# Kernel optimization log

Measured on AMD Instinct MI355X. Metric: run time of the kernel, lower is better.

Reference implementation:

```python
import jax, jax.numpy as jnp
import numpy as np
from jax import lax

B, L, H, K = 64, 1024, 768, 4
C1, C2 = 0.1, 0.1


def crf_marginals(feats, maskf, T):
    """Batched linear-chain CRF forward-backward.
    feats: [B,L,K] emission scores, maskf: [B,L] float (1=valid), T: [K,K] transitions.
    Returns marginals [B,L,K] (zeroed at padded positions)."""
    a0 = feats[:, 0]  # [B,K]

    def fwd_step(a, xs):
        f_t, m_t = xs  # [B,K], [B]
        new = f_t + jax.nn.logsumexp(a[:, :, None] + T[None], axis=1)
        a = jnp.where(m_t[:, None] > 0, new, a)  # freeze alpha past last valid token
        return a, a

    _, alphas_rest = lax.scan(fwd_step, a0,
                              (jnp.swapaxes(feats[:, 1:], 0, 1), maskf[:, 1:].T))
    alphas = jnp.concatenate([a0[None], alphas_rest], axis=0)  # [L,B,K]
    logZ = jax.nn.logsumexp(alphas[-1], axis=-1)  # [B] (alpha frozen at last valid t)

    bL = jnp.zeros_like(a0)

    def bwd_step(b, xs):
        f_n, m_n = xs  # emission/mask at t+1
        new = jax.nn.logsumexp(T[None] + (f_n + b)[:, None, :], axis=2)
        b = jnp.where(m_n[:, None] > 0, new, b)  # beta stays 0 until last valid token
        return b, b

    xs = (jnp.swapaxes(feats[:, 1:][:, ::-1], 0, 1), maskf[:, 1:][:, ::-1].T)
    _, betas_rev = lax.scan(bwd_step, bL, xs)
    betas = jnp.concatenate([bL[None], betas_rev], axis=0)[::-1]  # [L,B,K]

    marg = jnp.exp(alphas + betas - logZ[None, :, None]) * maskf.T[:, :, None]
    return jnp.swapaxes(marg, 0, 1)  # [B,L,K]


def _forward(hidden, maskf, w, b, T):
    feats = hidden @ w.T + b                      # [B,L,K] feat2tri
    marg = crf_marginals(feats, maskf, T)
    sp = marg[:, :, 1]                            # select_polarities, masked [B,L]
    gamma = sp.sum(axis=1) / 2.0                  # [B]
    sent_vs = jnp.einsum('bl,blh->bh', sp, hidden) / gamma[:, None]
    s_prob = sp / gamma[:, None]                  # padded-ragged per-token probs
    s_prob_norm = jnp.abs(s_prob).sum(axis=1).mean()
    pena = jax.nn.relu(T[1, 0] - T[0, 0]) + jax.nn.relu(T[0, 1] - T[1, 1])
    norm_pen = C1 * pena + C2 * s_prob_norm
    return sent_vs, norm_pen, s_prob


def setup_inputs():
    key = jax.random.key(0)
    ks = jax.random.split(key, 8)
    hidden = jax.random.normal(ks[0], (B, L, H), dtype=jnp.float32)
    seq_lens = jax.random.randint(ks[1], (B,), L // 4, L + 1)
    # hidden_mask: 0 for valid tokens, nonzero for padding (forward uses mask = hidden_mask==0)
    hidden_mask = (jnp.arange(L)[None, :] >= seq_lens[:, None]).astype(jnp.int32)
    subj_position = jax.random.randint(ks[2], (B, L), -20, 21)
    obj_position = jax.random.randint(ks[3], (B, L), -20, 21)
    pe_inputs = jax.random.randint(ks[4], (B, L), 0, 2 * L)
    pe_binary = jax.random.randint(ks[5], (B, L), 0, 2)
    w_feat2tri = jax.random.normal(ks[6], (K, H), dtype=jnp.float32) * (1.0 / np.sqrt(H)).astype(np.float32)
    b_feat2tri = jnp.zeros((K,), dtype=jnp.float32)
    transitions = jax.random.normal(ks[7], (K, K), dtype=jnp.float32) * 0.1
    return dict(hidden=hidden, hidden_mask=hidden_mask, subj_position=subj_position,
                obj_position=obj_position, seq_lens=seq_lens, pe_inputs=pe_inputs,
                pe_binary=pe_binary, w_feat2tri=w_feat2tri, b_feat2tri=b_feat2tri,
                transitions=transitions)


def reference(hidden, hidden_mask, subj_position, obj_position, seq_lens, pe_inputs,
              pe_binary, w_feat2tri, b_feat2tri, transitions):
    maskf = (hidden_mask == 0).astype(hidden.dtype)
    # relevance is computed in the original forward but never consumed downstream,
    # so it has no effect on outputs; omitted here.
    return _forward(hidden, maskf, w_feat2tri, b_feat2tri, transitions)
```

## Files before the change

### kernel.cpp

```cpp
#include <hip/hip_runtime.h>

#define B 64
#define L 1024
#define H 768
#define NROWS (B * L)
#define LOG2E 1.4426950408889634f
#define CS 16
#define NCH 64
#define NEG -1e30f

#define EXP2(x) __builtin_amdgcn_exp2f(x)
#define LOG2(x) __builtin_amdgcn_logf(x)

__device__ __forceinline__ void gbarrier(unsigned* cnt, unsigned nblk) {
    __syncthreads();
    if (threadIdx.x == 0) {
        __threadfence();
        __hip_atomic_fetch_add(cnt, 1u, __ATOMIC_ACQ_REL, __HIP_MEMORY_SCOPE_AGENT);
        while (__hip_atomic_load(cnt, __ATOMIC_ACQUIRE, __HIP_MEMORY_SCOPE_AGENT) < nblk)
            __builtin_amdgcn_s_sleep(1);
        __threadfence();
    }
    __syncthreads();
}

__global__ __launch_bounds__(256) void feats_kernel(
    const float* __restrict__ hidden, const float* __restrict__ w,
    const float* __restrict__ bias, float4* __restrict__ featsT,
    unsigned* __restrict__ counters)
{
    if (blockIdx.x == 0 && threadIdx.x < 4) counters[threadIdx.x] = 0u;

    const int lane = threadIdx.x & 63;
    const int wave = (blockIdx.x * blockDim.x + threadIdx.x) >> 6;
    const int nwaves = (gridDim.x * blockDim.x) >> 6;

    float wr[3][4][4];
#pragma unroll
    for (int c = 0; c < 3; ++c)
#pragma unroll
        for (int j = 0; j < 4; ++j)
#pragma unroll
            for (int k = 0; k < 4; ++k)
                wr[c][j][k] = w[k * H + lane * 4 + 256 * c + j];
    const float bb0 = bias[0], bb1 = bias[1], bb2 = bias[2], bb3 = bias[3];

    for (int row = wave; row < NROWS; row += nwaves) {
        const float4* hrow = reinterpret_cast<const float4*>(hidden) + (size_t)row * (H / 4);
        float acc[4] = {0.f, 0.f, 0.f, 0.f};
#pragma unroll
        for (int c = 0; c < 3; ++c) {
            float4 h = hrow[lane + 64 * c];
            const float hv[4] = {h.x, h.y, h.z, h.w};
#pragma unroll
            for (int j = 0; j < 4; ++j)
#pragma unroll
                for (int k = 0; k < 4; ++k)
                    acc[k] = fmaf(hv[j], wr[c][j][k], acc[k]);
        }
#pragma unroll
        for (int k = 0; k < 4; ++k) {
            float v = acc[k];
#pragma unroll
            for (int s = 32; s >= 1; s >>= 1) v += __shfl_xor(v, s, 64);
            acc[k] = v;
        }
        if (lane == 0) {
            const int b = row >> 10, l = row & 1023;
            featsT[l * B + b] = make_float4((acc[0] + bb0) * LOG2E, (acc[1] + bb1) * LOG2E,
                                            (acc[2] + bb2) * LOG2E, (acc[3] + bb3) * LOG2E);
        }
    }
}

__global__ __launch_bounds__(128) void crf_mid_kernel(
    const float4* __restrict__ featsT, const int* __restrict__ seq_lens,
    const float* __restrict__ T, float* __restrict__ mats,
    float* __restrict__ vbound, float* __restrict__ logZ,
    float* __restrict__ spu, float* __restrict__ chunksum,
    unsigned* __restrict__ counters)
{
    const int tid = threadIdx.x;
    const int b = tid & 63;
    const int dir = tid >> 6;
    const int c = blockIdx.x;
    const int sl = seq_lens[b];

    float eT2[4][4];
#pragma unroll
    for (int i = 0; i < 4; ++i)
#pragma unroll
        for (int j = 0; j < 4; ++j) eT2[i][j] = EXP2(T[i * 4 + j] * LOG2E);

    {
        const int lo = c * CS + 1;
        const int hi = min(c * CS + CS, L - 1);
        const int ns = hi - lo + 1;

        float4 fr[CS];
#pragma unroll
        for (int u = 0; u < CS; ++u) {
            const int t = dir ? max(hi - u, lo) : min(lo + u, hi);
            fr[u] = featsT[t * B + b];
        }

        float M[4][4];
#pragma unroll
        for (int i = 0; i < 4; ++i)
#pragma unroll
            for (int j = 0; j < 4; ++j) M[i][j] = (i == j) ? 0.f : NEG;

        if (dir == 0) {
#pragma unroll
            for (int u = 0; u < CS; ++u) {
                const int t = lo + u;
                const bool valid = (u < ns) && (t < sl);
                const float f[4] = {fr[u].x, fr[u].y, fr[u].z, fr[u].w};
                float nM[4][4];
#pragma unroll
                for (int i = 0; i < 4; ++i) {
                    const float rm = fmaxf(fmaxf(M[i][0], M[i][1]), fmaxf(M[i][2], M[i][3]));
                    const float e0 = EXP2(M[i][0] - rm), e1 = EXP2(M[i][1] - rm);
                    const float e2 = EXP2(M[i][2] - rm), e3 = EXP2(M[i][3] - rm);
#pragma unroll
                    for (int j = 0; j < 4; ++j) {
                        const float s = (e0 * eT2[0][j] + e1 * eT2[1][j]) + (e2 * eT2[2][j] + e3 * eT2[3][j]);
                        nM[i][j] = f[j] + rm + LOG2(s);
                    }
                }
#pragma unroll
                for (int i = 0; i < 4; ++i)
#pragma unroll
                    for (int j = 0; j < 4; ++j) M[i][j] = valid ? nM[i][j] : M[i][j];
            }
        } else {
#pragma unroll
            for (int u = 0; u < CS; ++u) {
                const int n = hi - u;
                const bool valid = (u < ns) && (n < sl);
                const float f[4] = {fr[u].x, fr[u].y, fr[u].z, fr[u].w};
                float nM[4][4];
#pragma unroll
                for (int j = 0; j < 4; ++j) {
                    const float c0 = f[0] + M[0][j], c1 = f[1] + M[1][j];
                    const float c2 = f[2] + M[2][j], c3 = f[3] + M[3][j];
                    const float cm = fmaxf(fmaxf(c0, c1), fmaxf(c2, c3));
                    const float g0 = EXP2(c0 - cm), g1 = EXP2(c1 - cm);
                    const float g2 = EXP2(c2 - cm), g3 = EXP2(c3 - cm);
#pragma unroll
                    for (int i = 0; i < 4; ++i) {
                        const float s = (g0 * eT2[i][0] + g1 * eT2[i][1]) + (g2 * eT2[i][2] + g3 * eT2[i][3]);
                        nM[i][j] = cm + LOG2(s);
                    }
                }
#pragma unroll
                for (int i = 0; i < 4; ++i)
#pragma unroll
                    for (int j = 0; j < 4; ++j) M[i][j] = valid ? nM[i][j] : M[i][j];
            }
        }
#pragma unroll
        for (int i = 0; i < 4; ++i)
#pragma unroll
            for (int j = 0; j < 4; ++j)
                mats[((dir * NCH + c) * 16 + i * 4 + j) * B + b] = M[i][j];
    }

    gbarrier(&counters[0], NCH);

    if (blockIdx.x == 0) {
        float Ms[8][16];
#pragma unroll
        for (int p = 0; p < 7; ++p) {
            const int cc = dir ? (NCH - 1 - p) : p;
#pragma unroll
            for (int k = 0; k < 16; ++k)
                Ms[p][k] = mats[((dir * NCH + cc) * 16 + k) * B + b];
        }

        float v0, v1, v2, v3;
        if (dir == 0) {
            const float4 f0 = featsT[b];
            v0 = f0.x; v1 = f0.y; v2 = f0.z; v3 = f0.w;
        } else {
            v0 = v1 = v2 = v3 = 0.f;
        }

#pragma unroll
        for (int u = 0; u < NCH; ++u) {
            const int cc = dir ? (NCH - 1 - u) : u;
            vbound[((dir * NCH + cc) * 4 + 0) * B + b] = v0;
            vbound[((dir * NCH + cc) * 4 + 1) * B + b] = v1;
            vbound[((dir * NCH + cc) * 4 + 2) * B + b] = v2;
            vbound[((dir * NCH + cc) * 4 + 3) * B + b] = v3;
            if (u + 7 < NCH) {
                const int cp = dir ? (NCH - 1 - (u + 7)) : (u + 7);
#pragma unroll
                for (int k = 0; k < 16; ++k)
                    Ms[(u + 7) & 7][k] = mats[((dir * NCH + cp) * 16 + k) * B + b];
            }
            float n[4];
            if (dir == 0) {
#pragma unroll
                for (int j = 0; j < 4; ++j) {
                    const float c0 = v0 + Ms[u & 7][0 * 4 + j], c1 = v1 + Ms[u & 7][1 * 4 + j];
                    const float c2 = v2 + Ms[u & 7][2 * 4 + j], c3 = v3 + Ms[u & 7][3 * 4 + j];
                    const float m = fmaxf(fmaxf(c0, c1), fmaxf(c2, c3));
                    const float s = (EXP2(c0 - m) + EXP2(c1 - m)) + (EXP2(c2 - m) + EXP2(c3 - m));
                    n[j] = m + LOG2(s);
                }
            } else {
#pragma unroll
                for (int i = 0; i < 4; ++i) {
                    const float c0 = v0 + Ms[u & 7][i * 4 + 0], c1 = v1 + Ms[u & 7][i * 4 + 1];
                    const float c2 = v2 + Ms[u & 7][i * 4 + 2], c3 = v3 + Ms[u & 7][i * 4 + 3];
                    const float m = fmaxf(fmaxf(c0, c1), fmaxf(c2, c3));
                    const float s = (EXP2(c0 - m) + EXP2(c1 - m)) + (EXP2(c2 - m) + EXP2(c3 - m));
                    n[i] = m + LOG2(s);
                }
            }
            v0 = n[0]; v1 = n[1]; v2 = n[2]; v3 = n[3];
        }
        if (dir == 0) {
            const float m = fmaxf(fmaxf(v0, v1), fmaxf(v2, v3));
            logZ[b] = m + LOG2(EXP2(v0 - m) + EXP2(v1 - m) + EXP2(v2 - m) + EXP2(v3 - m));
        }
    }

    gbarrier(&counters[1], NCH);

    __shared__ float ldb[CS * 64];
    {
        const int base = c * CS;

        if (dir == 1) {
            float v0 = vbound[((NCH + c) * 4 + 0) * B + b];
            float v1 = vbound[((NCH + c) * 4 + 1) * B + b];
            float v2 = vbound[((NCH + c) * 4 + 2) * B + b];
            float v3 = vbound[((NCH + c) * 4 + 3) * B + b];
            const bool last = (c == NCH - 1);
            const int hi_n = last ? (L - 1) : (base + CS);
            const int cnt = last ? (CS - 1) : CS;
            if (last) ldb[15 * 64 + b] = v1;
            float4 fr[CS];
#pragma unroll
            for (int u = 0; u < CS; ++u) fr[u] = featsT[max(hi_n - u, base + 1) * B + b];
#pragma unroll
            for (int u = 0; u < CS; ++u) {
                if (u < cnt) {
                    const int n = hi_n - u;
                    const bool valid = n < sl;
                    const float4 f = fr[u];
                    const float c0 = f.x + v0, c1 = f.y + v1, c2 = f.z + v2, c3 = f.w + v3;
                    const float m = fmaxf(fmaxf(c0, c1), fmaxf(c2, c3));
                    const float g0 = EXP2(c0 - m), g1 = EXP2(c1 - m), g2 = EXP2(c2 - m), g3 = EXP2(c3 - m);
                    const float s0 = (g0 * eT2[0][0] + g1 * eT2[0][1]) + (g2 * eT2[0][2] + g3 * eT2[0][3]);
                    const float s1 = (g0 * eT2[1][0] + g1 * eT2[1][1]) + (g2 * eT2[1][2] + g3 * eT2[1][3]);
                    const float s2 = (g0 * eT2[2][0] + g1 * eT2[2][1]) + (g2 * eT2[2][2] + g3 * eT2[2][3]);
                    const float s3 = (g0 * eT2[3][0] + g1 * eT2[3][1]) + (g2 * eT2[3][2] + g3 * eT2[3][3]);
                    const float n0 = m + LOG2(s0), n1 = m + LOG2(s1);
                    const float n2 = m + LOG2(s2), n3 = m + LOG2(s3);
                    v0 = valid ? n0 : v0; v1 = valid ? n1 : v1;
                    v2 = valid ? n2 : v2; v3 = valid ? n3 : v3;
                    ldb[(n - 1 - base) * 64 + b] = v1;
                }
            }
        }

        float av[CS];
        if (dir == 0) {
            float a0 = vbound[(c * 4 + 0) * B + b];
            float a1 = vbound[(c * 4 + 1) * B + b];
            float a2 = vbound[(c * 4 + 2) * B + b];
            float a3 = vbound[(c * 4 + 3) * B + b];
            av[0] = a1;
            float4 fr[CS - 1];
#pragma unroll
            for (int u = 1; u < CS; ++u) fr[u - 1] = featsT[(c * CS + u) * B + b];
#pragma unroll
            for (int u = 1; u < CS; ++u) {
                const int t = base + u;
                const bool valid = t < sl;
                const float4 f = fr[u - 1];
                const float m = fmaxf(fmaxf(a0, a1), fmaxf(a2, a3));
                const float e0 = EXP2(a0 - m), e1 = EXP2(a1 - m), e2 = EXP2(a2 - m), e3 = EXP2(a3 - m);
                const float s0 = (e0 * eT2[0][0] + e1 * eT2[1][0]) + (e2 * eT2[2][0] + e3 * eT2[3][0]);
                const float s1 = (e0 * eT2[0][1] + e1 * eT2[1][1]) + (e2 * eT2[2][1] + e3 * eT2[3][1]);
                const float s2 = (e0 * eT2[0][2] + e1 * eT2[1][2]) + (e2 * eT2[2][2] + e3 * eT2[3][2]);
                const float s3 = (e0 * eT2[0][3] + e1 * eT2[1][3]) + (e2 * eT2[2][3] + e3 * eT2[3][3]);
                const float n0 = f.x + m + LOG2(s0), n1 = f.y + m + LOG2(s1);
                const float n2 = f.z + m + LOG2(s2), n3 = f.w + m + LOG2(s3);
                a0 = valid ? n0 : a0; a1 = valid ? n1 : a1;
                a2 = valid ? n2 : a2; a3 = valid ? n3 : a3;
                av[u] = a1;
            }
        }

        __syncthreads();

        if (dir == 0) {
            const float lz = logZ[b];
            float sp[CS];
            float local = 0.f;
#pragma unroll
            for (int u = 0; u < CS; ++u) {
                const int l = base + u;
                const float x = (l < sl) ? EXP2(av[u] + ldb[u * 64 + b] - lz) : 0.f;
                sp[u] = x;
                local += x;
            }
            float4* dst = reinterpret_cast<float4*>(spu + b * L + base);
#pragma unroll
            for (int q = 0; q < 4; ++q)
                dst[q] = make_float4(sp[4 * q], sp[4 * q + 1], sp[4 * q + 2], sp[4 * q + 3]);
            chunksum[c * 64 + b] = local;
        }
    }
}

__global__ __launch_bounds__(256) void sentv_kernel(
    const float* __restrict__ hidden, const float* __restrict__ spu,
    const float* __restrict__ chunksum, const float* __restrict__ T,
    float* __restrict__ out, float* __restrict__ sprob)
{
    const int hc = blockIdx.x;
    const int b  = blockIdx.y;
    const int tid = threadIdx.x;
    const int lane = tid & 63;
    const int w = tid >> 6;

    __shared__ float s_tot;
    if (tid < 64) {
        float v = chunksum[tid * 64 + b];
#pragma unroll
        for (int s = 32; s >= 1; s >>= 1) v += __shfl_xor(v, s, 64);
        if (tid == 0) s_tot = v;
    }
    __syncthreads();
    const float inv = 2.0f / s_tot;

    const float4* hb = reinterpret_cast<const float4*>(hidden + ((size_t)b * L) * H + hc * 256) + lane;
    const float* sp = spu + b * L;

    float4 acc = make_float4(0.f, 0.f, 0.f, 0.f);
#pragma unroll 8
    for (int i = 0; i < 256; ++i) {
        const int l = w + 4 * i;
        const float s = sp[l];
        const float4 h = hb[(size_t)l * (H / 4)];
        acc.x = fmaf(s, h.x, acc.x); acc.y = fmaf(s, h.y, acc.y);
        acc.z = fmaf(s, h.z, acc.z); acc.w = fmaf(s, h.w, acc.w);
    }

    __shared__ float4 red[4][64];
    red[w][lane] = acc;
    __syncthreads();
    if (tid < 64) {
        const float4 a0 = red[0][lane], a1 = red[1][lane], a2 = red[2][lane], a3 = red[3][lane];
        float4 r;
        r.x = ((a0.x + a1.x) + (a2.x + a3.x)) * inv;
        r.y = ((a0.y + a1.y) + (a2.y + a3.y)) * inv;
        r.z = ((a0.z + a1.z) + (a2.z + a3.z)) * inv;
        r.w = ((a0.w + a1.w) + (a2.w + a3.w)) * inv;
        reinterpret_cast<float4*>(out + (size_t)b * H + hc * 256)[lane] = r;
    }

    if (hc == 0) {
#pragma unroll
        for (int q = 0; q < 4; ++q) {
            const int l = tid + q * 256;
            sprob[b * L + l] = sp[l] * inv;
        }
        if (b == 0 && tid == 0) {
            const float pena = fmaxf(T[4] - T[0], 0.f) + fmaxf(T[1] - T[5], 0.f);
            out[B * H] = 0.1f * pena + 0.1f * 2.0f;
        }
    }
}

extern "C" void kernel_launch(void* const* d_in, const int* in_sizes, int n_in,
                              void* d_out, int out_size, void* d_ws, size_t ws_size,
                              hipStream_t stream) {
    const float* hidden   = (const float*)d_in[0];
    const int*   seq_lens = (const int*)d_in[4];
    const float* w        = (const float*)d_in[7];
    const float* bias     = (const float*)d_in[8];
    const float* T        = (const float*)d_in[9];

    float* ws = (float*)d_ws;
    float4*   featsT   = (float4*)(ws);
    float*    mats     = ws + 262144;
    float*    vbound   = ws + 393216;
    float*    logZ     = ws + 425984;
    float*    chunksum = ws + 426048;
    float*    spu      = ws + 430144;
    unsigned* counters = (unsigned*)(ws + 495680);

    float* out   = (float*)d_out;
    float* sprob = out + B * H + 1;

    feats_kernel<<<2048, 256, 0, stream>>>(hidden, w, bias, featsT, counters);
    crf_mid_kernel<<<NCH, 128, 0, stream>>>((const float4*)featsT, seq_lens, T, mats,
                                            vbound, logZ, spu, chunksum, counters);
    sentv_kernel<<<dim3(3, 64), 256, 0, stream>>>(hidden, spu, chunksum, T, out, sprob);
}
```

Measured before the change: 107.0 us.

## Switch CRF to scaled probability space, split kernels, and re-grid sentence-vector reduction

The CRF scans now run in linear probability space with periodic power-of-two renormalisation, which replaces log-sum-exp (many exp2/log2 per step) with plain multiply-adds. The single fused CRF kernel and its software grid barriers are split into separate chunk-matrix, boundary, and rescan launches. The weighted hidden reduction is re-gridded to 512 blocks of 768 threads with a separate final combine kernel, to raise parallelism when streaming hidden. The cost is three extra kernel launches and a risk of precision or underflow differences from scaled-linear arithmetic.

```diff
diff --git a/kernel.cpp b/kernel.cpp
--- a/kernel.cpp
+++ b/kernel.cpp
@@ -7,30 +7,22 @@
 #define LOG2E 1.4426950408889634f
 #define CS 16
 #define NCH 64
-#define NEG -1e30f
 
 #define EXP2(x) __builtin_amdgcn_exp2f(x)
 #define LOG2(x) __builtin_amdgcn_logf(x)
 
-__device__ __forceinline__ void gbarrier(unsigned* cnt, unsigned nblk) {
-    __syncthreads();
-    if (threadIdx.x == 0) {
-        __threadfence();
-        __hip_atomic_fetch_add(cnt, 1u, __ATOMIC_ACQ_REL, __HIP_MEMORY_SCOPE_AGENT);
-        while (__hip_atomic_load(cnt, __ATOMIC_ACQUIRE, __HIP_MEMORY_SCOPE_AGENT) < nblk)
-            __builtin_amdgcn_s_sleep(1);
-        __threadfence();
-    }
-    __syncthreads();
+__device__ __forceinline__ void renorm4(float& x0, float& x1, float& x2, float& x3, float& lc) {
+    const float g = fmaxf(fmaxf(x0, x1), fmaxf(x2, x3));
+    const int e = (__float_as_int(g) >> 23) & 255;
+    const float s = __int_as_float((254 - e) << 23);
+    x0 *= s; x1 *= s; x2 *= s; x3 *= s;
+    lc += (float)(e - 127);
 }
 
 __global__ __launch_bounds__(256) void feats_kernel(
     const float* __restrict__ hidden, const float* __restrict__ w,
-    const float* __restrict__ bias, float4* __restrict__ featsT,
-    unsigned* __restrict__ counters)
-{
-    if (blockIdx.x == 0 && threadIdx.x < 4) counters[threadIdx.x] = 0u;
-
+    const float* __restrict__ bias, float4* __restrict__ pfeatsT)
+{
     const int lane = threadIdx.x & 63;
     const int wave = (blockIdx.x * blockDim.x + threadIdx.x) >> 6;
     const int nwaves = (gridDim.x * blockDim.x) >> 6;
@@ -67,24 +59,177 @@
         }
         if (lane == 0) {
             const int b = row >> 10, l = row & 1023;
-            featsT[l * B + b] = make_float4((acc[0] + bb0) * LOG2E, (acc[1] + bb1) * LOG2E,
-                                            (acc[2] + bb2) * LOG2E, (acc[3] + bb3) * LOG2E);
-        }
-    }
-}
-
-__global__ __launch_bounds__(128) void crf_mid_kernel(
-    const float4* __restrict__ featsT, const int* __restrict__ seq_lens,
-    const float* __restrict__ T, float* __restrict__ mats,
-    float* __restrict__ vbound, float* __restrict__ logZ,
-    float* __restrict__ spu, float* __restrict__ chunksum,
-    unsigned* __restrict__ counters)
+            pfeatsT[l * B + b] = make_float4(EXP2((acc[0] + bb0) * LOG2E),
+                                             EXP2((acc[1] + bb1) * LOG2E),
+                                             EXP2((acc[2] + bb2) * LOG2E),
+                                             EXP2((acc[3] + bb3) * LOG2E));
+        }
+    }
+}
+
+__global__ __launch_bounds__(128) void chunkmat_kernel(
+    const float4* __restrict__ pfeatsT, const int* __restrict__ seq_lens,
+    const float* __restrict__ T, float* __restrict__ mats_p,
+    float* __restrict__ mats_lc)
+{
+    const int b = threadIdx.x & 63;
+    const int dir = threadIdx.x >> 6;
+    const int c = blockIdx.x;
+    const int sl = seq_lens[b];
+    const int lo = c * CS + 1;
+    const int hi = min(c * CS + CS, L - 1);
+    const int ns = hi - lo + 1;
+
+    float eT2[4][4];
+#pragma unroll
+    for (int i = 0; i < 4; ++i)
+#pragma unroll
+        for (int j = 0; j < 4; ++j) eT2[i][j] = EXP2(T[i * 4 + j] * LOG2E);
+
+    float4 fr[CS];
+#pragma unroll
+    for (int u = 0; u < CS; ++u) {
+        const int t = dir ? max(hi - u, lo) : min(lo + u, hi);
+        fr[u] = pfeatsT[t * B + b];
+    }
+
+    float M[4][4];
+#pragma unroll
+    for (int i = 0; i < 4; ++i)
+#pragma unroll
+        for (int j = 0; j < 4; ++j) M[i][j] = (i == j) ? 1.f : 0.f;
+    float lc = 0.f;
+
+#pragma unroll
+    for (int u = 0; u < CS; ++u) {
+        const int pos = dir ? (hi - u) : (lo + u);
+        const bool valid = (u < ns) && (pos < sl);
+        const float f[4] = {fr[u].x, fr[u].y, fr[u].z, fr[u].w};
+        float nM[4][4];
+        if (dir == 0) {
+#pragma unroll
+            for (int i = 0; i < 4; ++i)
+#pragma unroll
+                for (int j = 0; j < 4; ++j) {
+                    const float s = (M[i][0] * eT2[0][j] + M[i][1] * eT2[1][j]) +
+                                    (M[i][2] * eT2[2][j] + M[i][3] * eT2[3][j]);
+                    nM[i][j] = s * f[j];
+                }
+        } else {
+            float Mg[4][4];
+#pragma unroll
+            for (int k = 0; k < 4; ++k)
+#pragma unroll
+                for (int j = 0; j < 4; ++j) Mg[k][j] = f[k] * M[k][j];
+#pragma unroll
+            for (int i = 0; i < 4; ++i)
+#pragma unroll
+                for (int j = 0; j < 4; ++j)
+                    nM[i][j] = (eT2[i][0] * Mg[0][j] + eT2[i][1] * Mg[1][j]) +
+                               (eT2[i][2] * Mg[2][j] + eT2[i][3] * Mg[3][j]);
+        }
+#pragma unroll
+        for (int i = 0; i < 4; ++i)
+#pragma unroll
+            for (int j = 0; j < 4; ++j) M[i][j] = valid ? nM[i][j] : M[i][j];
+
+        if (u == 7 || u == CS - 1) {
+            float g = 0.f;
+#pragma unroll
+            for (int i = 0; i < 4; ++i)
+#pragma unroll
+                for (int j = 0; j < 4; ++j) g = fmaxf(g, M[i][j]);
+            const int e = (__float_as_int(g) >> 23) & 255;
+            const float s = __int_as_float((254 - e) << 23);
+#pragma unroll
+            for (int i = 0; i < 4; ++i)
+#pragma unroll
+                for (int j = 0; j < 4; ++j) M[i][j] *= s;
+            lc += (float)(e - 127);
+        }
+    }
+#pragma unroll
+    for (int i = 0; i < 4; ++i)
+#pragma unroll
+        for (int j = 0; j < 4; ++j)
+            mats_p[((dir * NCH + c) * 16 + i * 4 + j) * B + b] = M[i][j];
+    mats_lc[(dir * NCH + c) * B + b] = lc;
+}
+
+__global__ __launch_bounds__(128) void bound_kernel(
+    const float4* __restrict__ pfeatsT, const float* __restrict__ mats_p,
+    const float* __restrict__ mats_lc, float* __restrict__ vbound_p,
+    float* __restrict__ vbound_lc, float* __restrict__ logZ)
+{
+    const int b = threadIdx.x & 63;
+    const int dir = threadIdx.x >> 6;
+
+    float Ms[8][17];
+#pragma unroll
+    for (int p = 0; p < 7; ++p) {
+        const int cc = dir ? (NCH - 1 - p) : p;
+#pragma unroll
+        for (int k = 0; k < 16; ++k)
+            Ms[p][k] = mats_p[((dir * NCH + cc) * 16 + k) * B + b];
+        Ms[p][16] = mats_lc[(dir * NCH + cc) * B + b];
+    }
+
+    float v0, v1, v2, v3, vlc = 0.f;
+    if (dir == 0) {
+        const float4 f0 = pfeatsT[b];
+        v0 = f0.x; v1 = f0.y; v2 = f0.z; v3 = f0.w;
+    } else {
+        v0 = v1 = v2 = v3 = 1.f;
+    }
+
+#pragma unroll 8
+    for (int u = 0; u < NCH; ++u) {
+        const int cc = dir ? (NCH - 1 - u) : u;
+        vbound_p[((dir * NCH + cc) * 4 + 0) * B + b] = v0;
+        vbound_p[((dir * NCH + cc) * 4 + 1) * B + b] = v1;
+        vbound_p[((dir * NCH + cc) * 4 + 2) * B + b] = v2;
+        vbound_p[((dir * NCH + cc) * 4 + 3) * B + b] = v3;
+        vbound_lc[(dir * NCH + cc) * B + b] = vlc;
+        if (u + 7 < NCH) {
+            const int cp = dir ? (NCH - 1 - (u + 7)) : (u + 7);
+#pragma unroll
+            for (int k = 0; k < 16; ++k)
+                Ms[(u + 7) & 7][k] = mats_p[((dir * NCH + cp) * 16 + k) * B + b];
+            Ms[(u + 7) & 7][16] = mats_lc[(dir * NCH + cp) * B + b];
+        }
+        const float* Pm = Ms[u & 7];
+        float n0, n1, n2, n3;
+        if (dir == 0) {
+            n0 = (v0 * Pm[0] + v1 * Pm[4]) + (v2 * Pm[8] + v3 * Pm[12]);
+            n1 = (v0 * Pm[1] + v1 * Pm[5]) + (v2 * Pm[9] + v3 * Pm[13]);
+            n2 = (v0 * Pm[2] + v1 * Pm[6]) + (v2 * Pm[10] + v3 * Pm[14]);
+            n3 = (v0 * Pm[3] + v1 * Pm[7]) + (v2 * Pm[11] + v3 * Pm[15]);
+        } else {
+            n0 = (Pm[0] * v0 + Pm[1] * v1) + (Pm[2] * v2 + Pm[3] * v3);
+            n1 = (Pm[4] * v0 + Pm[5] * v1) + (Pm[6] * v2 + Pm[7] * v3);
+            n2 = (Pm[8] * v0 + Pm[9] * v1) + (Pm[10] * v2 + Pm[11] * v3);
+            n3 = (Pm[12] * v0 + Pm[13] * v1) + (Pm[14] * v2 + Pm[15] * v3);
+        }
+        v0 = n0; v1 = n1; v2 = n2; v3 = n3;
+        vlc += Pm[16];
+        renorm4(v0, v1, v2, v3, vlc);
+    }
+    if (dir == 0)
+        logZ[b] = LOG2(((v0 + v1) + (v2 + v3))) + vlc;
+}
+
+__global__ __launch_bounds__(128) void rescan_sp_kernel(
+    const float4* __restrict__ pfeatsT, const int* __restrict__ seq_lens,
+    const float* __restrict__ T, const float* __restrict__ vbound_p,
+    const float* __restrict__ vbound_lc, const float* __restrict__ logZ,
+    float* __restrict__ spu, float* __restrict__ chunksum)
 {
     const int tid = threadIdx.x;
     const int b = tid & 63;
     const int dir = tid >> 6;
     const int c = blockIdx.x;
     const int sl = seq_lens[b];
+    const int base = c * CS;
 
     float eT2[4][4];
 #pragma unroll
@@ -92,242 +237,137 @@
 #pragma unroll
         for (int j = 0; j < 4; ++j) eT2[i][j] = EXP2(T[i * 4 + j] * LOG2E);
 
-    {
-        const int lo = c * CS + 1;
-        const int hi = min(c * CS + CS, L - 1);
-        const int ns = hi - lo + 1;
-
+    __shared__ float ldb_p[CS * 64];
+    __shared__ float ldb_lc[CS * 64];
+
+    if (dir == 1) {
+        float v0 = vbound_p[((NCH + c) * 4 + 0) * B + b];
+        float v1 = vbound_p[((NCH + c) * 4 + 1) * B + b];
+        float v2 = vbound_p[((NCH + c) * 4 + 2) * B + b];
+        float v3 = vbound_p[((NCH + c) * 4 + 3) * B + b];
+        float blc = vbound_lc[(NCH + c) * B + b];
+        const bool last = (c == NCH - 1);
+        const int hi_n = last ? (L - 1) : (base + CS);
+        const int cnt = last ? (CS - 1) : CS;
+        if (last) { ldb_p[15 * 64 + b] = v1; ldb_lc[15 * 64 + b] = blc; }
         float4 fr[CS];
 #pragma unroll
+        for (int u = 0; u < CS; ++u) fr[u] = pfeatsT[max(hi_n - u, base + 1) * B + b];
+#pragma unroll
         for (int u = 0; u < CS; ++u) {
-            const int t = dir ? max(hi - u, lo) : min(lo + u, hi);
-            fr[u] = featsT[t * B + b];
-        }
-
-        float M[4][4];
-#pragma unroll
-        for (int i = 0; i < 4; ++i)
-#pragma unroll
-            for (int j = 0; j < 4; ++j) M[i][j] = (i == j) ? 0.f : NEG;
-
-        if (dir == 0) {
-#pragma unroll
-            for (int u = 0; u < CS; ++u) {
-                const int t = lo + u;
-                const bool valid = (u < ns) && (t < sl);
-                const float f[4] = {fr[u].x, fr[u].y, fr[u].z, fr[u].w};
-                float nM[4][4];
-#pragma unroll
-                for (int i = 0; i < 4; ++i) {
-                    const float rm = fmaxf(fmaxf(M[i][0], M[i][1]), fmaxf(M[i][2], M[i][3]));
-                    const float e0 = EXP2(M[i][0] - rm), e1 = EXP2(M[i][1] - rm);
-                    const float e2 = EXP2(M[i][2] - rm), e3 = EXP2(M[i][3] - rm);
-#pragma unroll
-                    for (int j = 0; j < 4; ++j) {
-                        const float s = (e0 * eT2[0][j] + e1 * eT2[1][j]) + (e2 * eT2[2][j] + e3 * eT2[3][j]);
-                        nM[i][j] = f[j] + rm + LOG2(s);
-                    }
-                }
-#pragma unroll
-                for (int i = 0; i < 4; ++i)
-#pragma unroll
-                    for (int j = 0; j < 4; ++j) M[i][j] = valid ? nM[i][j] : M[i][j];
+            if (u < cnt) {
+                const int n = hi_n - u;
+                const bool valid = n < sl;
+                const float4 f = fr[u];
+                const float c0 = f.x * v0, c1 = f.y * v1, c2 = f.z * v2, c3 = f.w * v3;
+                const float n0 = (eT2[0][0] * c0 + eT2[0][1] * c1) + (eT2[0][2] * c2 + eT2[0][3] * c3);
+                const float n1 = (eT2[1][0] * c0 + eT2[1][1] * c1) + (eT2[1][2] * c2 + eT2[1][3] * c3);
+                const float n2 = (eT2[2][0] * c0 + eT2[2][1] * c1) + (eT2[2][2] * c2 + eT2[2][3] * c3);
+                const float n3 = (eT2[3][0] * c0 + eT2[3][1] * c1) + (eT2[3][2] * c2 + eT2[3][3] * c3);
+                v0 = valid ? n0 : v0; v1 = valid ? n1 : v1;
+                v2 = valid ? n2 : v2; v3 = valid ? n3 : v3;
+                if ((u & 3) == 3) renorm4(v0, v1, v2, v3, blc);
+                ldb_p[(n - 1 - base) * 64 + b] = v1;
+                ldb_lc[(n - 1 - base) * 64 + b] = blc;
             }
-        } else {
-#pragma unroll
-            for (int u = 0; u < CS; ++u) {
-                const int n = hi - u;
-                const bool valid = (u < ns) && (n < sl);
-                const float f[4] = {fr[u].x, fr[u].y, fr[u].z, fr[u].w};
-                float nM[4][4];
-#pragma unroll
-                for (int j = 0; j < 4; ++j) {
-                    const float c0 = f[0] + M[0][j], c1 = f[1] + M[1][j];
-                    const float c2 = f[2] + M[2][j], c3 = f[3] + M[3][j];
-                    const float cm = fmaxf(fmaxf(c0, c1), fmaxf(c2, c3));
-                    const float g0 = EXP2(c0 - cm), g1 = EXP2(c1 - cm);
-                    const float g2 = EXP2(c2 - cm), g3 = EXP2(c3 - cm);
-#pragma unroll
-                    for (int i = 0; i < 4; ++i) {
-                        const float s = (g0 * eT2[i][0] + g1 * eT2[i][1]) + (g2 * eT2[i][2] + g3 * eT2[i][3]);
-                        nM[i][j] = cm + LOG2(s);
-                    }
-                }
-#pragma unroll
-                for (int i = 0; i < 4; ++i)
-#pragma unroll
-                    for (int j = 0; j < 4; ++j) M[i][j] = valid ? nM[i][j] : M[i][j];
-            }
-        }
-#pragma unroll
-        for (int i = 0; i < 4; ++i)
-#pragma unroll
-            for (int j = 0; j < 4; ++j)
-                mats[((dir * NCH + c) * 16 + i * 4 + j) * B + b] = M[i][j];
-    }
-
-    gbarrier(&counters[0], NCH);
-
-    if (blockIdx.x == 0) {
-        float Ms[8][16];
-#pragma unroll
-        for (int p = 0; p < 7; ++p) {
-            const int cc = dir ? (NCH - 1 - p) : p;
-#pragma unroll
-            for (int k = 0; k < 16; ++k)
-                Ms[p][k] = mats[((dir * NCH + cc) * 16 + k) * B + b];
-        }
-
-        float v0, v1, v2, v3;
-        if (dir == 0) {
-            const float4 f0 = featsT[b];
-            v0 = f0.x; v1 = f0.y; v2 = f0.z; v3 = f0.w;
-        } else {
-            v0 = v1 = v2 = v3 = 0.f;
-        }
-
-#pragma unroll
-        for (int u = 0; u < NCH; ++u) {
-            const int cc = dir ? (NCH - 1 - u) : u;
-            vbound[((dir * NCH + cc) * 4 + 0) * B + b] = v0;
-            vbound[((dir * NCH + cc) * 4 + 1) * B + b] = v1;
-            vbound[((dir * NCH + cc) * 4 + 2) * B + b] = v2;
-            vbound[((dir * NCH + cc) * 4 + 3) * B + b] = v3;
-            if (u + 7 < NCH) {
-                const int cp = dir ? (NCH - 1 - (u + 7)) : (u + 7);
-#pragma unroll
-                for (int k = 0; k < 16; ++k)
-                    Ms[(u + 7) & 7][k] = mats[((dir * NCH + cp) * 16 + k) * B + b];
-            }
-            float n[4];
-            if (dir == 0) {
-#pragma unroll
-                for (int j = 0; j < 4; ++j) {
-                    const float c0 = v0 + Ms[u & 7][0 * 4 + j], c1 = v1 + Ms[u & 7][1 * 4 + j];
-                    const float c2 = v2 + Ms[u & 7][2 * 4 + j], c3 = v3 + Ms[u & 7][3 * 4 + j];
-                    const float m = fmaxf(fmaxf(c0, c1), fmaxf(c2, c3));
-                    const float s = (EXP2(c0 - m) + EXP2(c1 - m)) + (EXP2(c2 - m) + EXP2(c3 - m));
-                    n[j] = m + LOG2(s);
-                }
-            } else {
-#pragma unroll
-                for (int i = 0; i < 4; ++i) {
-                    const float c0 = v0 + Ms[u & 7][i * 4 + 0], c1 = v1 + Ms[u & 7][i * 4 + 1];
-                    const float c2 = v2 + Ms[u & 7][i * 4 + 2], c3 = v3 + Ms[u & 7][i * 4 + 3];
-                    const float m = fmaxf(fmaxf(c0, c1), fmaxf(c2, c3));
-                    const float s = (EXP2(c0 - m) + EXP2(c1 - m)) + (EXP2(c2 - m) + EXP2(c3 - m));
-                    n[i] = m + LOG2(s);
-                }
-            }
-            v0 = n[0]; v1 = n[1]; v2 = n[2]; v3 = n[3];
-        }
-        if (dir == 0) {
-            const float m = fmaxf(fmaxf(v0, v1), fmaxf(v2, v3));
-            logZ[b] = m + LOG2(EXP2(v0 - m) + EXP2(v1 - m) + EXP2(v2 - m) + EXP2(v3 - m));
-        }
-    }
-
-    gbarrier(&counters[1], NCH);
-
-    __shared__ float ldb[CS * 64];
-    {
-        const int base = c * CS;
-
-        if (dir == 1) {
-            float v0 = vbound[((NCH + c) * 4 + 0) * B + b];
-            float v1 = vbound[((NCH + c) * 4 + 1) * B + b];
-            float v2 = vbound[((NCH + c) * 4 + 2) * B + b];
-            float v3 = vbound[((NCH + c) * 4 + 3) * B + b];
-            const bool last = (c == NCH - 1);
-            const int hi_n = last ? (L - 1) : (base + CS);
-            const int cnt = last ? (CS - 1) : CS;
-            if (last) ldb[15 * 64 + b] = v1;
-            float4 fr[CS];
-#pragma unroll
-            for (int u = 0; u < CS; ++u) fr[u] = featsT[max(hi_n - u, base + 1) * B + b];
-#pragma unroll
-            for (int u = 0; u < CS; ++u) {
-                if (u < cnt) {
-                    const int n = hi_n - u;
-                    const bool valid = n < sl;
-                    const float4 f = fr[u];
-                    const float c0 = f.x + v0, c1 = f.y + v1, c2 = f.z + v2, c3 = f.w + v3;
-                    const float m = fmaxf(fmaxf(c0, c1), fmaxf(c2, c3));
-                    const float g0 = EXP2(c0 - m), g1 = EXP2(c1 - m), g2 = EXP2(c2 - m), g3 = EXP2(c3 - m);
-                    const float s0 = (g0 * eT2[0][0] + g1 * eT2[0][1]) + (g2 * eT2[0][2] + g3 * eT2[0][3]);
-                    const float s1 = (g0 * eT2[1][0] + g1 * eT2[1][1]) + (g2 * eT2[1][2] + g3 * eT2[1][3]);
-                    const float s2 = (g0 * eT2[2][0] + g1 * eT2[2][1]) + (g2 * eT2[2][2] + g3 * eT2[2][3]);
-                    const float s3 = (g0 * eT2[3][0] + g1 * eT2[3][1]) + (g2 * eT2[3][2] + g3 * eT2[3][3]);
-                    const float n0 = m + LOG2(s0), n1 = m + LOG2(s1);
-                    const float n2 = m + LOG2(s2), n3 = m + LOG2(s3);
-                    v0 = valid ? n0 : v0; v1 = valid ? n1 : v1;
-                    v2 = valid ? n2 : v2; v3 = valid ? n3 : v3;
-                    ldb[(n - 1 - base) * 64 + b] = v1;
-                }
-            }
-        }
-
-        float av[CS];
-        if (dir == 0) {
-            float a0 = vbound[(c * 4 + 0) * B + b];
-            float a1 = vbound[(c * 4 + 1) * B + b];
-            float a2 = vbound[(c * 4 + 2) * B + b];
-            float a3 = vbound[(c * 4 + 3) * B + b];
-            av[0] = a1;
-            float4 fr[CS - 1];
-#pragma unroll
-            for (int u = 1; u < CS; ++u) fr[u - 1] = featsT[(c * CS + u) * B + b];
-#pragma unroll
-            for (int u = 1; u < CS; ++u) {
-                const int t = base + u;
-                const bool valid = t < sl;
-                const float4 f = fr[u - 1];
-                const float m = fmaxf(fmaxf(a0, a1), fmaxf(a2, a3));
-                const float e0 = EXP2(a0 - m), e1 = EXP2(a1 - m), e2 = EXP2(a2 - m), e3 = EXP2(a3 - m);
-                const float s0 = (e0 * eT2[0][0] + e1 * eT2[1][0]) + (e2 * eT2[2][0] + e3 * eT2[3][0]);
-                const float s1 = (e0 * eT2[0][1] + e1 * eT2[1][1]) + (e2 * eT2[2][1] + e3 * eT2[3][1]);
-                const float s2 = (e0 * eT2[0][2] + e1 * eT2[1][2]) + (e2 * eT2[2][2] + e3 * eT2[3][2]);
-                const float s3 = (e0 * eT2[0][3] + e1 * eT2[1][3]) + (e2 * eT2[2][3] + e3 * eT2[3][3]);
-                const float n0 = f.x + m + LOG2(s0), n1 = f.y + m + LOG2(s1);
-                const float n2 = f.z + m + LOG2(s2), n3 = f.w + m + LOG2(s3);
-                a0 = valid ? n0 : a0; a1 = valid ? n1 : a1;
-                a2 = valid ? n2 : a2; a3 = valid ? n3 : a3;
-                av[u] = a1;
-            }
-        }
-
-        __syncthreads();
-
-        if (dir == 0) {
-            const float lz = logZ[b];
-            float sp[CS];
-            float local = 0.f;
-#pragma unroll
-            for (int u = 0; u < CS; ++u) {
-                const int l = base + u;
-                const float x = (l < sl) ? EXP2(av[u] + ldb[u * 64 + b] - lz) : 0.f;
-                sp[u] = x;
-                local += x;
-            }
-            float4* dst = reinterpret_cast<float4*>(spu + b * L + base);
-#pragma unroll
-            for (int q = 0; q < 4; ++q)
-                dst[q] = make_float4(sp[4 * q], sp[4 * q + 1], sp[4 * q + 2], sp[4 * q + 3]);
-            chunksum[c * 64 + b] = local;
-        }
-    }
-}
-
-__global__ __launch_bounds__(256) void sentv_kernel(
+        }
+    }
+
+    float av_p[CS], av_lc[CS];
+    if (dir == 0) {
+        float a0 = vbound_p[(c * 4 + 0) * B + b];
+        float a1 = vbound_p[(c * 4 + 1) * B + b];
+        float a2 = vbound_p[(c * 4 + 2) * B + b];
+        float a3 = vbound_p[(c * 4 + 3) * B + b];
+        float alc = vbound_lc[c * B + b];
+        av_p[0] = a1; av_lc[0] = alc;
+        float4 fr[CS - 1];
+#pragma unroll
+        for (int u = 1; u < CS; ++u) fr[u - 1] = pfeatsT[(base + u) * B + b];
+#pragma unroll
+        for (int u = 1; u < CS; ++u) {
+            const int t = base + u;
+            const bool valid = t < sl;
+            const float4 f = fr[u - 1];
+            const float s0 = (a0 * eT2[0][0] + a1 * eT2[1][0]) + (a2 * eT2[2][0] + a3 * eT2[3][0]);
+            const float s1 = (a0 * eT2[0][1] + a1 * eT2[1][1]) + (a2 * eT2[2][1] + a3 * eT2[3][1]);
+            const float s2 = (a0 * eT2[0][2] + a1 * eT2[1][2]) + (a2 * eT2[2][2] + a3 * eT2[3][2]);
+            const float s3 = (a0 * eT2[0][3] + a1 * eT2[1][3]) + (a2 * eT2[2][3] + a3 * eT2[3][3]);
+            const float n0 = s0 * f.x, n1 = s1 * f.y, n2 = s2 * f.z, n3 = s3 * f.w;
+            a0 = valid ? n0 : a0; a1 = valid ? n1 : a1;
+            a2 = valid ? n2 : a2; a3 = valid ? n3 : a3;
+            if ((u & 3) == 3) renorm4(a0, a1, a2, a3, alc);
+            av_p[u] = a1; av_lc[u] = alc;
+        }
+    }
+
+    __syncthreads();
+
+    if (dir == 0) {
+        const float lz = logZ[b];
+        float sp[CS];
+        float local = 0.f;
+#pragma unroll
+        for (int u = 0; u < CS; ++u) {
+            const int l = base + u;
+            const float x = (l < sl)
+                ? av_p[u] * ldb_p[u * 64 + b] * EXP2(av_lc[u] + ldb_lc[u * 64 + b] - lz)
+                : 0.f;
+            sp[u] = x;
+            local += x;
+        }
+        float4* dst = reinterpret_cast<float4*>(spu + b * L + base);
+#pragma unroll
+        for (int q = 0; q < 4; ++q)
+            dst[q] = make_float4(sp[4 * q], sp[4 * q + 1], sp[4 * q + 2], sp[4 * q + 3]);
+        chunksum[c * 64 + b] = local;
+    }
+}
+
+__global__ __launch_bounds__(768) void sentv_kernel(
     const float* __restrict__ hidden, const float* __restrict__ spu,
-    const float* __restrict__ chunksum, const float* __restrict__ T,
+    float4* __restrict__ partial)
+{
+    const int b  = blockIdx.x >> 3;
+    const int lc = blockIdx.x & 7;
+    const int tid = threadIdx.x;
+    const int col = tid % 192;
+    const int r   = tid / 192;
+
+    const float4* hb = reinterpret_cast<const float4*>(hidden) + ((size_t)b * L + lc * 128) * 192;
+    const float* sp = spu + b * L + lc * 128;
+
+    float4 acc = make_float4(0.f, 0.f, 0.f, 0.f);
+#pragma unroll 4
+    for (int i = 0; i < 32; ++i) {
+        const int l = 4 * i + r;
+        const float s = sp[l];
+        const float4 h = hb[(size_t)l * 192 + col];
+        acc.x = fmaf(s, h.x, acc.x); acc.y = fmaf(s, h.y, acc.y);
+        acc.z = fmaf(s, h.z, acc.z); acc.w = fmaf(s, h.w, acc.w);
+    }
+
+    __shared__ float4 red[768];
+    red[tid] = acc;
+    __syncthreads();
+    if (tid < 192) {
+        const float4 a0 = red[tid], a1 = red[tid + 192], a2 = red[tid + 384], a3 = red[tid + 576];
+        float4 rr;
+        rr.x = (a0.x + a1.x) + (a2.x + a3.x);
+        rr.y = (a0.y + a1.y) + (a2.y + a3.y);
+        rr.z = (a0.z + a1.z) + (a2.z + a3.z);
+        rr.w = (a0.w + a1.w) + (a2.w + a3.w);
+        partial[((size_t)lc * B + b) * 192 + tid] = rr;
+    }
+}
+
+__global__ __launch_bounds__(256) void final_kernel(
+    const float4* __restrict__ partial, const float* __restrict__ chunksum,
+    const float* __restrict__ spu, const float* __restrict__ T,
     float* __restrict__ out, float* __restrict__ sprob)
 {
-    const int hc = blockIdx.x;
-    const int b  = blockIdx.y;
+    const int b = blockIdx.x;
     const int tid = threadIdx.x;
-    const int lane = tid & 63;
-    const int w = tid >> 6;
 
     __shared__ float s_tot;
     if (tid < 64) {
@@ -339,42 +379,25 @@
     __syncthreads();
     const float inv = 2.0f / s_tot;
 
-    const float4* hb = reinterpret_cast<const float4*>(hidden + ((size_t)b * L) * H + hc * 256) + lane;
-    const float* sp = spu + b * L;
-
-    float4 acc = make_float4(0.f, 0.f, 0.f, 0.f);
-#pragma unroll 8
-    for (int i = 0; i < 256; ++i) {
-        const int l = w + 4 * i;
-        const float s = sp[l];
-        const float4 h = hb[(size_t)l * (H / 4)];
-        acc.x = fmaf(s, h.x, acc.x); acc.y = fmaf(s, h.y, acc.y);
-        acc.z = fmaf(s, h.z, acc.z); acc.w = fmaf(s, h.w, acc.w);
-    }
-
-    __shared__ float4 red[4][64];
-    red[w][lane] = acc;
-    __syncthreads();
-    if (tid < 64) {
-        const float4 a0 = red[0][lane], a1 = red[1][lane], a2 = red[2][lane], a3 = red[3][lane];
-        float4 r;
-        r.x = ((a0.x + a1.x) + (a2.x + a3.x)) * inv;
-        r.y = ((a0.y + a1.y) + (a2.y + a3.y)) * inv;
-        r.z = ((a0.z + a1.z) + (a2.z + a3.z)) * inv;
-        r.w = ((a0.w + a1.w) + (a2.w + a3.w)) * inv;
-        reinterpret_cast<float4*>(out + (size_t)b * H + hc * 256)[lane] = r;
-    }
-
-    if (hc == 0) {
-#pragma unroll
-        for (int q = 0; q < 4; ++q) {
-            const int l = tid + q * 256;
-            sprob[b * L + l] = sp[l] * inv;
-        }
-        if (b == 0 && tid == 0) {
-            const float pena = fmaxf(T[4] - T[0], 0.f) + fmaxf(T[1] - T[5], 0.f);
-            out[B * H] = 0.1f * pena + 0.1f * 2.0f;
-        }
+    if (tid < 192) {
+        float4 acc = make_float4(0.f, 0.f, 0.f, 0.f);
+#pragma unroll
+        for (int q = 0; q < 8; ++q) {
+            const float4 p = partial[((size_t)q * B + b) * 192 + tid];
+            acc.x += p.x; acc.y += p.y; acc.z += p.z; acc.w += p.w;
+        }
+        acc.x *= inv; acc.y *= inv; acc.z *= inv; acc.w *= inv;
+        reinterpret_cast<float4*>(out + (size_t)b * H)[tid] = acc;
+    }
+
+#pragma unroll
+    for (int q = 0; q < 4; ++q) {
+        const int l = tid + q * 256;
+        sprob[b * L + l] = spu[b * L + l] * inv;
+    }
+    if (b == 0 && tid == 0) {
+        const float pena = fmaxf(T[4] - T[0], 0.f) + fmaxf(T[1] - T[5], 0.f);
+        out[B * H] = 0.1f * pena + 0.1f * 2.0f;
     }
 }
 
@@ -388,19 +411,25 @@
     const float* T        = (const float*)d_in[9];
 
     float* ws = (float*)d_ws;
-    float4*   featsT   = (float4*)(ws);
-    float*    mats     = ws + 262144;
-    float*    vbound   = ws + 393216;
-    float*    logZ     = ws + 425984;
-    float*    chunksum = ws + 426048;
-    float*    spu      = ws + 430144;
-    unsigned* counters = (unsigned*)(ws + 495680);
+    float4* pfeatsT    = (float4*)(ws);
+    float*  mats_p     = ws + 262144;
+    float*  mats_lc    = ws + 393216;
+    float*  vbound_p   = ws + 401408;
+    float*  vbound_lc  = ws + 434176;
+    float*  logZ       = ws + 442368;
+    float*  chunksum   = ws + 442432;
+    float*  spu        = ws + 446528;
+    float4* partial    = (float4*)(ws + 512064);
 
     float* out   = (float*)d_out;
     float* sprob = out + B * H + 1;
 
-    feats_kernel<<<2048, 256, 0, stream>>>(hidden, w, bias, featsT, counters);
-    crf_mid_kernel<<<NCH, 128, 0, stream>>>((const float4*)featsT, seq_lens, T, mats,
-                                            vbound, logZ, spu, chunksum, counters);
-    sentv_kernel<<<dim3(3, 64), 256, 0, stream>>>(hidden, spu, chunksum, T, out, sprob);
-}
+    feats_kernel<<<2048, 256, 0, stream>>>(hidden, w, bias, pfeatsT);
+    chunkmat_kernel<<<NCH, 128, 0, stream>>>((const float4*)pfeatsT, seq_lens, T, mats_p, mats_lc);
+    bound_kernel<<<1, 128, 0, stream>>>((const float4*)pfeatsT, mats_p, mats_lc,
+                                        vbound_p, vbound_lc, logZ);
+    rescan_sp_kernel<<<NCH, 128, 0, stream>>>((const float4*)pfeatsT, seq_lens, T,
+                                              vbound_p, vbound_lc, logZ, spu, chunksum);
+    sentv_kernel<<<512, 768, 0, stream>>>(hidden, spu, partial);
+    final_kernel<<<64, 256, 0, stream>>>(partial, chunksum, spu, T, out, sprob);
+}
```

Result: slower. 112.6 us (+5.2%).
